# Kernel tuning notes

Hardware: AMD Instinct MI355X
Metric: run time of the kernel (lower is better)

The kernel has to match this reference:

```python
import jax, jax.numpy as jnp
import numpy as np
from jax import lax

B, C, H, W = 8, 512, 64, 64
COUT, K = 512, 3
STYLE_DIM = 512


def setup_inputs() -> dict:
    key = jax.random.key(0)
    k1, k2, k3, k4, k5 = jax.random.split(key, 5)
    x = jax.random.normal(k1, (B, C, H, W), dtype=jnp.float32)
    style = jax.random.normal(k2, (B, STYLE_DIM), dtype=jnp.float32)
    # conv weight (OIHW), scaled like a typical init
    weight = jax.random.normal(k3, (COUT, C, K, K), dtype=jnp.float32) * (1.0 / np.sqrt(C * K * K))
    # modulation Linear: style_dim -> in_channels
    mod_w = jax.random.normal(k4, (C, STYLE_DIM), dtype=jnp.float32) * (1.0 / np.sqrt(STYLE_DIM))
    mod_b = jnp.ones((C,), dtype=jnp.float32) + 0.01 * jax.random.normal(k5, (C,), dtype=jnp.float32)
    return {"x": x, "style": style, "weight": weight, "mod_w": mod_w, "mod_b": mod_b}


def reference(x, style, weight, mod_w, mod_b):
    # s = modulation(style): Linear, shape (B, C) -> per-sample per-channel scale
    s = style @ mod_w.T + mod_b  # (B, C)
    xm = x * s[:, :, None, None]  # modulate input (B, C, H, W)
    # The torch code runs conv2d(groups=B) with weight.repeat(B,1,1,1); since the
    # weight is identical per group this equals a plain batched conv.
    y = lax.conv_general_dilated(
        xm, weight,
        window_strides=(1, 1),
        padding=[(1, 1), (1, 1)],
        rhs_dilation=(1, 1),
        dimension_numbers=("NCHW", "OIHW", "NCHW"),
    )  # (B, COUT, H, W)
    return y
```

## Files before the change

kernel.cpp:

```cpp
#include <hip/hip_runtime.h>
#include <cstdint>
#include <cstddef>

typedef short s16x8 __attribute__((ext_vector_type(8)));
typedef float f32x16 __attribute__((ext_vector_type(16)));

#define WS_S     0
#define WS_ZERO  16384
#define WS_XQ    32768
#define XQ_BYTES (8 * 64 * 64 * 64 * 16)
#define WS_WQ    (WS_XQ + XQ_BYTES)
#define WQ_BYTES (4 * 32 * 9 * 2 * 128 * 8 * 2)
#define WS_NEEDED ((size_t)WS_WQ + (size_t)WQ_BYTES)

__device__ __forceinline__ short f2bf(float f) {
  unsigned u = __builtin_bit_cast(unsigned, f);
  unsigned r = (u + 0x7fffu + ((u >> 16) & 1u)) >> 16;
  return (short)r;
}

__device__ __forceinline__ void gload_lds16(const void* g, void* l) {
  __builtin_amdgcn_global_load_lds(
      (const __attribute__((address_space(1))) void*)g,
      (__attribute__((address_space(3))) void*)l, 16, 0, 0);
}

__global__ void k_style(const float* __restrict__ style,
                        const float* __restrict__ mod_w,
                        const float* __restrict__ mod_b,
                        float* __restrict__ s_out,
                        float* __restrict__ zb) {
  if (blockIdx.x == 0) zb[threadIdx.x] = 0.0f;
  int wave = threadIdx.x >> 6, lane = threadIdx.x & 63;
  int wid = blockIdx.x * 4 + wave;
  int b = wid >> 9, c = wid & 511;
  const float4* st = (const float4*)(style + b * 512);
  const float4* mw = (const float4*)(mod_w + c * 512);
  float4 a0 = st[lane * 2], a1 = st[lane * 2 + 1];
  float4 b0 = mw[lane * 2], b1 = mw[lane * 2 + 1];
  float sum = a0.x * b0.x + a0.y * b0.y + a0.z * b0.z + a0.w * b0.w +
              a1.x * b1.x + a1.y * b1.y + a1.z * b1.z + a1.w * b1.w;
  #pragma unroll
  for (int off = 32; off; off >>= 1) sum += __shfl_down(sum, off);
  if (lane == 0) s_out[b * 512 + c] = sum + mod_b[c];
}

__global__ void k_xq(const float* __restrict__ x, const float* __restrict__ s,
                     char* __restrict__ xq) {
  int t = blockIdx.x * 256 + threadIdx.x;
  int w = t & 63, cg = (t >> 6) & 63, h = (t >> 12) & 63, b = t >> 18;
  const float* xp = x + (((b * 512 + cg * 8) * 64 + h) * 64 + w);
  const float* sp = s + b * 512 + cg * 8;
  s16x8 v;
  #pragma unroll
  for (int j = 0; j < 8; ++j) v[j] = f2bf(xp[j * 4096] * sp[j]);
  *(s16x8*)(xq + (size_t)t * 16) = v;
}

__global__ void k_wq(const float* __restrict__ wt, char* __restrict__ wq) {
  int tap = blockIdx.x, ch = blockIdx.y, nb = blockIdx.z;
  int kg = threadIdx.x >> 7, n = threadIdx.x & 127;
  const float* wp = wt + ((size_t)(nb * 128 + n) * 512 + ch * 16 + kg * 8) * 9 + tap;
  s16x8 v;
  #pragma unroll
  for (int j = 0; j < 8; ++j) v[j] = f2bf(wp[j * 9]);
  size_t idx = ((size_t)(nb * 32 + ch) * 9 + tap) * 256 + kg * 128 + n;
  *(s16x8*)(wq + idx * 16) = v;
}

__global__ __launch_bounds__(512, 2) void k_conv(
    const char* __restrict__ xq, const char* __restrict__ wq,
    const char* __restrict__ zerob, float* __restrict__ out) {
  extern __shared__ char smem[];
  char* wt_base = smem;
  char* xs_base = smem + 73728;

  const int tid = threadIdx.x;
  const int lane = tid & 63, wave = tid >> 6;
  const int l5 = lane >> 5, l31 = lane & 31;
  const int wc = wave >> 2;
  const int wp = wave & 3;
  const int mb = blockIdx.x, nb = blockIdx.y;
  const int b = mb >> 3;
  const int row0 = (mb & 7) << 3;

  if (tid < 80) {
    int dbuf = tid / 40, q = tid % 40;
    int j = q >> 2, kg = (q >> 1) & 1, side = q & 1;
    s16x8 z = {0, 0, 0, 0, 0, 0, 0, 0};
    *(s16x8*)(xs_base + dbuf * 21120 + ((j * 2 + kg) * 66 + side * 65) * 16) = z;
  }

  f32x16 acc[2][4];
  #pragma unroll
  for (int i = 0; i < 2; ++i)
    #pragma unroll
    for (int j = 0; j < 4; ++j)
      #pragma unroll
      for (int e = 0; e < 16; ++e) acc[i][j][e] = 0.0f;

  const char* wq_base = wq + (size_t)nb * (32 * 36864) + lane * 16;
  const char* xq_base = xq + (size_t)b * 4194304 + lane * 16;

  const int a_off = l5 * 2048 + l31 * 16;
  const int b_off = l5 * 1056 + l31 * 16;
  const int xs_woff = wp * 4224;

  #define STAGE(buf, ch)                                                      \
    _Pragma("unroll")                                                         \
    for (int i = 0; i < 7; ++i) {                                             \
      int seg = wave * 7 + i;                        \
      if (seg < 36) {                                                         \
        gload_lds16(wq_base + (size_t)(ch) * 36864 + seg * 1024,              \
                    wt_base + (buf) * 36864 + seg * 1024);                    \
      } else {                                                                \
        int q = seg - 36, j = q >> 1, kg = q & 1;                             \
        int h = row0 - 1 + j;                                                 \
        const char* src = (h >= 0 && h < 64)                                  \
            ? xq_base + (size_t)(h * 64 + (ch) * 2 + kg) * 1024               \
            : zerob + lane * 16;                                              \
        gload_lds16(src, xs_base + (buf) * 21120 + ((j * 2 + kg) * 66 + 1) * 16); \
      }                                                                       \
    }

  STAGE(0, 0);
  __syncthreads();

  for (int ch = 0; ch < 32; ++ch) {
    const int cur = ch & 1;
    if (ch < 31) STAGE(cur ^ 1, ch + 1);

    const char* wt = wt_base + cur * 36864;
    const char* xs_w = xs_base + cur * 21120 + xs_woff;

    #pragma unroll
    for (int kw = 0; kw < 3; ++kw) {
      s16x8 bC[4][2];
      #pragma unroll
      for (int r4 = 0; r4 < 4; ++r4)
        #pragma unroll
        for (int chh = 0; chh < 2; ++chh)
          bC[r4][chh] = *(const s16x8*)(xs_w + (r4 * 132 + chh * 32 + kw) * 16 + b_off);
      #pragma unroll
      for (int kh = 0; kh < 3; ++kh) {
        const int tap = kh * 3 + kw;
        s16x8 afr[2];
        #pragma unroll
        for (int ct = 0; ct < 2; ++ct)
          afr[ct] = *(const s16x8*)(wt + tap * 4096 + (wc * 2 + ct) * 512 + a_off);
        #pragma unroll
        for (int ct = 0; ct < 2; ++ct)
          #pragma unroll
          for (int pt = 0; pt < 4; ++pt)
            acc[ct][pt] = __builtin_amdgcn_mfma_f32_32x32x16_bf16(
                afr[ct], bC[(pt >> 1) + kh][pt & 1], acc[ct][pt], 0, 0, 0);
      }
    }
    __syncthreads();
  }

  #pragma unroll
  for (int ct = 0; ct < 2; ++ct) {
    #pragma unroll
    for (int pt = 0; pt < 4; ++pt) {
      int h = row0 + wp * 2 + (pt >> 1);
      int w = (pt & 1) * 32 + l31;
      int cb = nb * 128 + wc * 64 + ct * 32 + 4 * l5;
      #pragma unroll
      for (int rg = 0; rg < 16; ++rg) {
        int cout = cb + (rg & 3) + 8 * (rg >> 2);
        out[((size_t)(b * 512 + cout) * 4096) + h * 64 + w] = acc[ct][pt][rg];
      }
    }
  }
  #undef STAGE
}

__global__ void k_naive(const float* __restrict__ x, const float* __restrict__ style,
                        const float* __restrict__ wt, const float* __restrict__ mw,
                        const float* __restrict__ mb_, float* __restrict__ out) {
  __shared__ float s_sh[512];
  int h = blockIdx.x, co = blockIdx.y, b = blockIdx.z, w = threadIdx.x;
  for (int c = w; c < 512; c += 64) {
    float a = mb_[c];
    for (int k = 0; k < 512; ++k) a += style[b * 512 + k] * mw[c * 512 + k];
    s_sh[c] = a;
  }
  __syncthreads();
  float acc = 0.0f;
  for (int c = 0; c < 512; ++c) {
    float sc = s_sh[c];
    const float* wp = wt + ((size_t)co * 512 + c) * 9;
    for (int kh = 0; kh < 3; ++kh) {
      int hy = h + kh - 1;
      if (hy < 0 || hy >= 64) continue;
      for (int kw = 0; kw < 3; ++kw) {
        int wx = w + kw - 1;
        if (wx < 0 || wx >= 64) continue;
        acc += wp[kh * 3 + kw] * x[((size_t)(b * 512 + c) * 64 + hy) * 64 + wx] * sc;
      }
    }
  }
  out[((size_t)(b * 512 + co) * 64 + h) * 64 + w] = acc;
}

extern "C" void kernel_launch(void* const* d_in, const int* in_sizes, int n_in,
                              void* d_out, int out_size, void* d_ws, size_t ws_size,
                              hipStream_t stream) {
  const float* x      = (const float*)d_in[0];
  const float* style  = (const float*)d_in[1];
  const float* weight = (const float*)d_in[2];
  const float* mod_w  = (const float*)d_in[3];
  const float* mod_b  = (const float*)d_in[4];
  float* out = (float*)d_out;
  char* ws = (char*)d_ws;

  if (ws_size >= WS_NEEDED) {
    float* s  = (float*)(ws + WS_S);
    float* zb = (float*)(ws + WS_ZERO);
    char* xq  = ws + WS_XQ;
    char* wq  = ws + WS_WQ;
    k_style<<<1024, 256, 0, stream>>>(style, mod_w, mod_b, s, zb);
    k_xq<<<8192, 256, 0, stream>>>(x, s, xq);
    k_wq<<<dim3(9, 32, 4), 256, 0, stream>>>(weight, wq);
    k_conv<<<dim3(64, 4), 512, 115968, stream>>>(xq, wq, (const char*)zb, out);
  } else {
    k_naive<<<dim3(64, 512, 8), 64, 0, stream>>>(x, style, weight, mod_w, mod_b, out);
  }
}
```

Before: 154.0 us.

## Fuse style, activation and weight prep kernels into one; raise MFMA wave priority

Merges the style linear, the modulate-and-quantize pass over x, and the weight bf16 repack into a single preprocessing launch. Each x block recomputes the 32 style scales it needs into shared memory. This removes two kernel launches and the round trip of s through global memory, at the cost of redundant style dot products (each scale computed 64 times, once per row). It also raises wave priority around the MFMA cluster in the conv loop to favour matrix issue over the loads.

```diff
diff --git a/kernel.cpp b/kernel.cpp
--- a/kernel.cpp
+++ b/kernel.cpp
@@ -5,8 +5,7 @@
 typedef short s16x8 __attribute__((ext_vector_type(8)));
 typedef float f32x16 __attribute__((ext_vector_type(16)));
 
-#define WS_S     0
-#define WS_ZERO  16384
+#define WS_ZB    0
 #define WS_XQ    32768
 #define XQ_BYTES (8 * 64 * 64 * 64 * 16)
 #define WS_WQ    (WS_XQ + XQ_BYTES)
@@ -25,47 +24,56 @@
       (__attribute__((address_space(3))) void*)l, 16, 0, 0);
 }
 
-__global__ void k_style(const float* __restrict__ style,
-                        const float* __restrict__ mod_w,
-                        const float* __restrict__ mod_b,
-                        float* __restrict__ s_out,
-                        float* __restrict__ zb) {
-  if (blockIdx.x == 0) zb[threadIdx.x] = 0.0f;
-  int wave = threadIdx.x >> 6, lane = threadIdx.x & 63;
-  int wid = blockIdx.x * 4 + wave;
-  int b = wid >> 9, c = wid & 511;
-  const float4* st = (const float4*)(style + b * 512);
-  const float4* mw = (const float4*)(mod_w + c * 512);
-  float4 a0 = st[lane * 2], a1 = st[lane * 2 + 1];
-  float4 b0 = mw[lane * 2], b1 = mw[lane * 2 + 1];
-  float sum = a0.x * b0.x + a0.y * b0.y + a0.z * b0.z + a0.w * b0.w +
-              a1.x * b1.x + a1.y * b1.y + a1.z * b1.z + a1.w * b1.w;
-  #pragma unroll
-  for (int off = 32; off; off >>= 1) sum += __shfl_down(sum, off);
-  if (lane == 0) s_out[b * 512 + c] = sum + mod_b[c];
-}
-
-__global__ void k_xq(const float* __restrict__ x, const float* __restrict__ s,
-                     char* __restrict__ xq) {
-  int t = blockIdx.x * 256 + threadIdx.x;
-  int w = t & 63, cg = (t >> 6) & 63, h = (t >> 12) & 63, b = t >> 18;
-  const float* xp = x + (((b * 512 + cg * 8) * 64 + h) * 64 + w);
-  const float* sp = s + b * 512 + cg * 8;
-  s16x8 v;
-  #pragma unroll
-  for (int j = 0; j < 8; ++j) v[j] = f2bf(xp[j * 4096] * sp[j]);
-  *(s16x8*)(xq + (size_t)t * 16) = v;
-}
-
-__global__ void k_wq(const float* __restrict__ wt, char* __restrict__ wq) {
-  int tap = blockIdx.x, ch = blockIdx.y, nb = blockIdx.z;
-  int kg = threadIdx.x >> 7, n = threadIdx.x & 127;
-  const float* wp = wt + ((size_t)(nb * 128 + n) * 512 + ch * 16 + kg * 8) * 9 + tap;
-  s16x8 v;
-  #pragma unroll
-  for (int j = 0; j < 8; ++j) v[j] = f2bf(wp[j * 9]);
-  size_t idx = ((size_t)(nb * 32 + ch) * 9 + tap) * 256 + kg * 128 + n;
-  *(s16x8*)(wq + idx * 16) = v;
+__global__ void k_pre(const float* __restrict__ x,
+                      const float* __restrict__ style,
+                      const float* __restrict__ mod_w,
+                      const float* __restrict__ mod_b,
+                      const float* __restrict__ wt,
+                      char* __restrict__ xq, char* __restrict__ wq,
+                      float* __restrict__ zb) {
+  const int bid = blockIdx.x, tid = threadIdx.x;
+  if (bid < 8192) {
+    __shared__ float s_sh[32];
+    const int cg0 = (bid & 15) * 4;
+    const int h = (bid >> 4) & 63, b = bid >> 10;
+    const int c_local = tid >> 3, piece = tid & 7;
+    const int c = cg0 * 8 + c_local;
+    const float4* st = (const float4*)(style + b * 512 + piece * 64);
+    const float4* mw = (const float4*)(mod_w + (size_t)c * 512 + piece * 64);
+    float sum = 0.0f;
+    #pragma unroll
+    for (int i = 0; i < 16; ++i) {
+      float4 a = st[i], bb = mw[i];
+      sum += a.x * bb.x + a.y * bb.y + a.z * bb.z + a.w * bb.w;
+    }
+    sum += __shfl_xor(sum, 1);
+    sum += __shfl_xor(sum, 2);
+    sum += __shfl_xor(sum, 4);
+    if (piece == 0) s_sh[c_local] = sum + mod_b[c];
+    __syncthreads();
+    const int w = tid & 63, cgl = (tid >> 6) & 3;
+    const int cg = cg0 + cgl;
+    const float* xp = x + (((size_t)(b * 512 + cg * 8) * 64 + h) * 64 + w);
+    s16x8 v;
+    #pragma unroll
+    for (int j = 0; j < 8; ++j) v[j] = f2bf(xp[(size_t)j * 4096] * s_sh[cgl * 8 + j]);
+    *(s16x8*)(xq + ((size_t)bid * 256 + tid) * 16) = v;
+  } else {
+    const int q = bid - 8192;
+    if (q == 0 && tid < 64) {
+      float4 z = make_float4(0.f, 0.f, 0.f, 0.f);
+      ((float4*)zb)[tid] = z;
+    }
+    const int tap = q % 9, t2 = q / 9;
+    const int ch = t2 % 32, nb = t2 / 32;
+    const int kg = tid >> 7, n = tid & 127;
+    const float* wp = wt + ((size_t)(nb * 128 + n) * 512 + ch * 16 + kg * 8) * 9 + tap;
+    s16x8 v;
+    #pragma unroll
+    for (int j = 0; j < 8; ++j) v[j] = f2bf(wp[j * 9]);
+    size_t idx = ((size_t)(nb * 32 + ch) * 9 + tap) * 256 + kg * 128 + n;
+    *(s16x8*)(wq + idx * 16) = v;
+  }
 }
 
 __global__ __launch_bounds__(512, 2) void k_conv(
@@ -148,12 +156,14 @@
         #pragma unroll
         for (int ct = 0; ct < 2; ++ct)
           afr[ct] = *(const s16x8*)(wt + tap * 4096 + (wc * 2 + ct) * 512 + a_off);
+        __builtin_amdgcn_s_setprio(1);
         #pragma unroll
         for (int ct = 0; ct < 2; ++ct)
           #pragma unroll
           for (int pt = 0; pt < 4; ++pt)
             acc[ct][pt] = __builtin_amdgcn_mfma_f32_32x32x16_bf16(
                 afr[ct], bC[(pt >> 1) + kh][pt & 1], acc[ct][pt], 0, 0, 0);
+        __builtin_amdgcn_s_setprio(0);
       }
     }
     __syncthreads();
@@ -216,13 +226,10 @@
   char* ws = (char*)d_ws;
 
   if (ws_size >= WS_NEEDED) {
-    float* s  = (float*)(ws + WS_S);
-    float* zb = (float*)(ws + WS_ZERO);
+    float* zb = (float*)(ws + WS_ZB);
     char* xq  = ws + WS_XQ;
     char* wq  = ws + WS_WQ;
-    k_style<<<1024, 256, 0, stream>>>(style, mod_w, mod_b, s, zb);
-    k_xq<<<8192, 256, 0, stream>>>(x, s, xq);
-    k_wq<<<dim3(9, 32, 4), 256, 0, stream>>>(weight, wq);
+    k_pre<<<9344, 256, 0, stream>>>(x, style, mod_w, mod_b, weight, xq, wq, zb);
     k_conv<<<dim3(64, 4), 512, 115968, stream>>>(xq, wq, (const char*)zb, out);
   } else {
     k_naive<<<dim3(64, 512, 8), 64, 0, stream>>>(x, style, weight, mod_w, mod_b, out);
```

Result: slower. 250.4 us (+62.6%).
